# Performance work log

Measured on AMD Instinct MI355X. Metric: run time of the kernel, lower is better.

## Reference

```python
import jax, jax.numpy as jnp
import numpy as np

B, S, D, H, E, N = 4, 1024, 1024, 4096, 1024, 8


def setup_inputs() -> dict:
    key = jax.random.key(0)
    ks = jax.random.split(key, 5)
    x = jax.random.normal(ks[0], (B, S, D), jnp.float32)
    # Learned parameters (Linear weights stored as [in, out] for x @ W)
    Wg = jax.random.normal(ks[1], (D, N), jnp.float32) * 0.02
    bg = jnp.zeros((N,), jnp.float32)
    W1 = jax.random.normal(ks[2], (N, D, H), jnp.float32) * 0.02
    b1 = jnp.zeros((N, H), jnp.float32)
    W2 = jax.random.normal(ks[3], (N, H, E), jnp.float32) * 0.02
    b2 = jnp.zeros((N, E), jnp.float32)
    return {"x": x, "Wg": Wg, "bg": bg, "W1": W1, "b1": b1,
            "W2": W2, "b2": b2, "num_experts_per_tok": 2}


def reference(x, Wg, bg, W1, b1, W2, b2, num_experts_per_tok):
    # Gating: softmax over experts
    gate_probs = jax.nn.softmax(x @ Wg + bg, axis=-1)            # [B,S,N]
    n_exp = gate_probs.shape[-1]
    # Top-k routing mask (indices are distinct, so summed one-hots == scatter of 1.0)
    _, topk_idx = jax.lax.top_k(gate_probs, num_experts_per_tok)  # [B,S,k]
    mask = jax.nn.one_hot(topk_idx, n_exp, dtype=gate_probs.dtype).sum(axis=-2)  # [B,S,N]
    gated = gate_probs * mask
    # F.normalize(p=1): divide by max(L1-norm, eps)
    gated = gated / jnp.maximum(jnp.sum(jnp.abs(gated), axis=-1, keepdims=True), 1e-12)
    # Dense all-expert FFN (matches torch.stack over ModuleList)
    h = jax.nn.relu(jnp.einsum('bsd,ndh->bsnh', x, W1) + b1)      # [B,S,N,H]
    expert_out = jnp.einsum('bsnh,nhe->bsne', h, W2) + b2          # [B,S,N,E]
    out = jnp.einsum('bsn,bsne->bse', gated, expert_out)           # [B,S,E]
    # Auxiliary load-balancing stats
    tokens = float(x.shape[0] * x.shape[1])
    importance = gate_probs.sum(axis=(0, 1)) / tokens              # [N]
    load = mask.sum(axis=(0, 1)) / tokens                          # [N]
    lb_loss = (n_exp * (importance * load).sum()).astype(out.dtype)
    return out, lb_loss, importance, load
```

## Files before the change

kernel.cpp:

```cpp
#include <hip/hip_runtime.h>

#define TOKENS 4096
#define DDIM 1024
#define HDIM 4096
#define EDIM 1024
#define NEXP 8
#define SLOTS (TOKENS * 2)
#define OUT_MAIN ((size_t)TOKENS * EDIM)
#define NKC2 2
#define KCHUNK2 (HDIM / NKC2)

typedef __bf16 bf16_t;
typedef bf16_t bf16x8 __attribute__((ext_vector_type(8)));
typedef float f32x4 __attribute__((ext_vector_type(4)));

__device__ __forceinline__ unsigned short f32_to_bf16(float f) {
  union { float f; unsigned u; } v; v.f = f;
  unsigned r = v.u + 0x7FFFu + ((v.u >> 16) & 1u);
  return (unsigned short)(r >> 16);
}

__device__ __forceinline__ void gload_lds16(const void* g, void* l) {
  __builtin_amdgcn_global_load_lds(
      (__attribute__((address_space(1))) void*)(g),
      (__attribute__((address_space(3))) void*)(l), 16, 0, 0);
}

__global__ __launch_bounds__(256) void gate_kernel(
    const float* __restrict__ x, const float* __restrict__ Wg,
    const float* __restrict__ bg, unsigned short* __restrict__ xb,
    int2* __restrict__ tok_e, float2* __restrict__ tok_w,
    float* __restrict__ probs) {
  const int wave = threadIdx.x >> 6;
  const int lane = threadIdx.x & 63;
  const int t = blockIdx.x * 4 + wave;
  const float4* xr = reinterpret_cast<const float4*>(x + (size_t)t * DDIM);
  ushort4* xbr = reinterpret_cast<ushort4*>(xb + (size_t)t * DDIM);

  float acc[NEXP];
#pragma unroll
  for (int n = 0; n < NEXP; n++) acc[n] = 0.f;

#pragma unroll
  for (int i = 0; i < 4; i++) {
    int d4 = lane + 64 * i;
    float4 xv = xr[d4];
    ushort4 o;
    o.x = f32_to_bf16(xv.x); o.y = f32_to_bf16(xv.y);
    o.z = f32_to_bf16(xv.z); o.w = f32_to_bf16(xv.w);
    xbr[d4] = o;
    const float* wrow = Wg + (size_t)d4 * 4 * NEXP;
#pragma unroll
    for (int n = 0; n < NEXP; n++)
      acc[n] += xv.x * wrow[n] + xv.y * wrow[NEXP + n] +
                xv.z * wrow[2 * NEXP + n] + xv.w * wrow[3 * NEXP + n];
  }
#pragma unroll
  for (int n = 0; n < NEXP; n++)
#pragma unroll
    for (int m = 32; m > 0; m >>= 1) acc[n] += __shfl_xor(acc[n], m, 64);

  if (lane == 0) {
    float p[NEXP];
    float mx = -1e30f;
#pragma unroll
    for (int n = 0; n < NEXP; n++) { p[n] = acc[n] + bg[n]; mx = fmaxf(mx, p[n]); }
    float s = 0.f;
#pragma unroll
    for (int n = 0; n < NEXP; n++) { p[n] = expf(p[n] - mx); s += p[n]; }
    float inv = 1.f / s;
#pragma unroll
    for (int n = 0; n < NEXP; n++) { p[n] *= inv; probs[(size_t)t * NEXP + n] = p[n]; }
    int e1 = 0; float p1 = p[0];
#pragma unroll
    for (int n = 1; n < NEXP; n++) if (p[n] > p1) { p1 = p[n]; e1 = n; }
    int e2 = (e1 == 0) ? 1 : 0; float p2 = p[e2];
#pragma unroll
    for (int n = 0; n < NEXP; n++) if (n != e1 && p[n] > p2) { p2 = p[n]; e2 = n; }
    float denom = p1 + p2;
    tok_e[t] = make_int2(e1, e2);
    tok_w[t] = make_float2(p1 / denom, p2 / denom);
  }
}

__global__ __launch_bounds__(1024) void route_kernel(
    const int2* __restrict__ tok_e, const float2* __restrict__ tok_w,
    int* __restrict__ offs_g, int* __restrict__ counts_g,
    int* __restrict__ token_ids, float* __restrict__ slot_w) {
  __shared__ int cnt[NEXP];
  __shared__ int offs[NEXP + 1];
  __shared__ int cur[NEXP];
  const int tid = threadIdx.x;
  if (tid < NEXP) cnt[tid] = 0;
  __syncthreads();
  int2 e[4]; float2 w[4];
#pragma unroll
  for (int i = 0; i < 4; i++) {
    int t = tid + 1024 * i;
    e[i] = tok_e[t]; w[i] = tok_w[t];
    atomicAdd(&cnt[e[i].x], 1);
    atomicAdd(&cnt[e[i].y], 1);
  }
  __syncthreads();
  if (tid == 0) {
    int s = 0;
#pragma unroll
    for (int n = 0; n < NEXP; n++) { offs[n] = s; cur[n] = s; s += cnt[n]; }
    offs[NEXP] = s;
  }
  __syncthreads();
  if (tid < NEXP) { offs_g[tid] = offs[tid]; counts_g[tid] = cnt[tid]; }
  if (tid == 0) offs_g[NEXP] = offs[NEXP];
#pragma unroll
  for (int i = 0; i < 4; i++) {
    int t = tid + 1024 * i;
    int s0 = atomicAdd(&cur[e[i].x], 1);
    token_ids[s0] = t; slot_w[s0] = w[i].x;
    int s1 = atomicAdd(&cur[e[i].y], 1);
    token_ids[s1] = t; slot_w[s1] = w[i].y;
  }
}

__global__ __launch_bounds__(256) void transpose_convert_kernel(
    const float* __restrict__ src, unsigned short* __restrict__ dst, int R, int C) {
  __shared__ float tile[64][65];
  const size_t mat = (size_t)R * C;
  const float* s = src + (size_t)blockIdx.z * mat;
  unsigned short* d = dst + (size_t)blockIdx.z * mat;
  int c0 = blockIdx.x * 64, r0 = blockIdx.y * 64;
  int tx = threadIdx.x & 15, ty = threadIdx.x >> 4;
#pragma unroll
  for (int i = 0; i < 4; i++) {
    int row = ty + 16 * i;
    float4 v = *reinterpret_cast<const float4*>(&s[(size_t)(r0 + row) * C + c0 + tx * 4]);
    tile[row][tx * 4 + 0] = v.x;
    tile[row][tx * 4 + 1] = v.y;
    tile[row][tx * 4 + 2] = v.z;
    tile[row][tx * 4 + 3] = v.w;
  }
  __syncthreads();
#pragma unroll
  for (int i = 0; i < 4; i++) {
    int col = ty + 16 * i;
    ushort4 o;
    o.x = f32_to_bf16(tile[tx * 4 + 0][col]);
    o.y = f32_to_bf16(tile[tx * 4 + 1][col]);
    o.z = f32_to_bf16(tile[tx * 4 + 2][col]);
    o.w = f32_to_bf16(tile[tx * 4 + 3][col]);
    *reinterpret_cast<ushort4*>(&d[(size_t)(c0 + col) * R + r0 + tx * 4]) = o;
  }
}

__global__ __launch_bounds__(256) void gemm1_kernel(
    const unsigned short* __restrict__ xb, const unsigned short* __restrict__ w1t,
    const float* __restrict__ b1, const int* __restrict__ token_ids,
    const int* __restrict__ offs, unsigned short* __restrict__ h) {
  const int e = blockIdx.z;
  const int off0 = offs[e];
  const int ne = offs[e + 1] - off0;
  const int mt = blockIdx.y;
  if (mt * 128 >= ne) return;
  const int nt = blockIdx.x;

  __shared__ unsigned short As[2][128 * 64];
  __shared__ unsigned short Bs[2][128 * 64];

  const int tid = threadIdx.x;
  const int lane = tid & 63;
  const int wave = tid >> 6;
  const int wm = (wave >> 1) * 64;
  const int wn = (wave & 1) * 64;

  const int prow = tid >> 3;
  const int krow = (tid & 7) ^ (prow & 7);
  const unsigned short* gA[4];
  const unsigned short* gB[4];
  const unsigned short* wbase = w1t + (size_t)e * HDIM * DDIM;
#pragma unroll
  for (int j = 0; j < 4; j++) {
    int row = prow + j * 32;
    int slot = off0 + min(mt * 128 + row, ne - 1);
    gA[j] = xb + (size_t)token_ids[slot] * DDIM + krow * 8;
    gB[j] = wbase + (size_t)(nt * 128 + row) * DDIM + krow * 8;
  }

  f32x4 acc[4][4];
#pragma unroll
  for (int i = 0; i < 4; i++)
#pragma unroll
    for (int j = 0; j < 4; j++) acc[i][j] = (f32x4)(0.f);

  const int frow = lane & 15;
  const int q = lane >> 4;
  const int NK = DDIM / 64;

  auto stage = [&](int tt, int buf) {
#pragma unroll
    for (int j = 0; j < 4; j++) {
      gload_lds16(gA[j] + tt * 64, &As[buf][j * 2048 + wave * 512]);
      gload_lds16(gB[j] + tt * 64, &Bs[buf][j * 2048 + wave * 512]);
    }
  };

  stage(0, 0);
  stage(1, 1);

  for (int t = 0; t < NK; t++) {
    const int cur = t & 1;
    if (t == NK - 1) asm volatile("s_waitcnt vmcnt(0)" ::: "memory");
    else             asm volatile("s_waitcnt vmcnt(8)" ::: "memory");
    __builtin_amdgcn_s_barrier();

    bf16x8 af[2][4], bfv[2][4];
#pragma unroll
    for (int kk = 0; kk < 2; kk++) {
#pragma unroll
      for (int mi = 0; mi < 4; mi++) {
        int row = wm + mi * 16 + frow;
        int k16 = (kk * 4 + q) ^ (row & 7);
        af[kk][mi] = *reinterpret_cast<const bf16x8*>(&As[cur][row * 64 + k16 * 8]);
      }
#pragma unroll
      for (int ni = 0; ni < 4; ni++) {
        int row = wn + ni * 16 + frow;
        int k16 = (kk * 4 + q) ^ (row & 7);
        bfv[kk][ni] = *reinterpret_cast<const bf16x8*>(&Bs[cur][row * 64 + k16 * 8]);
      }
    }
    asm volatile("s_waitcnt lgkmcnt(0)" ::: "memory");
    __builtin_amdgcn_s_barrier();
    if (t + 2 < NK) stage(t + 2, cur);

    __builtin_amdgcn_s_setprio(1);
#pragma unroll
    for (int kk = 0; kk < 2; kk++)
#pragma unroll
      for (int mi = 0; mi < 4; mi++)
#pragma unroll
        for (int ni = 0; ni < 4; ni++)
          acc[mi][ni] = __builtin_amdgcn_mfma_f32_16x16x32_bf16(af[kk][mi], bfv[kk][ni], acc[mi][ni], 0, 0, 0);
    __builtin_amdgcn_s_setprio(0);
  }

  const float* b1e = b1 + (size_t)e * HDIM + nt * 128;
  const int r4 = (lane >> 4) * 4;
  const int cb = lane & 15;
#pragma unroll
  for (int mi = 0; mi < 4; mi++) {
#pragma unroll
    for (int r = 0; r < 4; r++) {
      int grow = mt * 128 + wm + mi * 16 + r4 + r;
      if (grow < ne) {
        unsigned short* hr = h + (size_t)(off0 + grow) * HDIM + nt * 128;
#pragma unroll
        for (int ni = 0; ni < 4; ni++) {
          int col = wn + ni * 16 + cb;
          float v = acc[mi][ni][r] + b1e[col];
          hr[col] = f32_to_bf16(fmaxf(v, 0.f));
        }
      }
    }
  }
}

__global__ __launch_bounds__(256) void gemm2_kernel(
    const unsigned short* __restrict__ h, const unsigned short* __restrict__ w2t,
    const float* __restrict__ b2, const int* __restrict__ token_ids,
    const float* __restrict__ slot_w, const int* __restrict__ offs,
    float* __restrict__ out) {
  const int ez = blockIdx.z;
  const int e = ez >> 1;
  const int kc = ez & 1;
  const int off0 = offs[e];
  const int ne = offs[e + 1] - off0;
  const int mt = blockIdx.y;
  if (mt * 128 >= ne) return;
  const int nt = blockIdx.x;

  __shared__ unsigned short As[2][128 * 64];
  __shared__ unsigned short Bs[2][128 * 64];

  const int tid = threadIdx.x;
  const int lane = tid & 63;
  const int wave = tid >> 6;
  const int wm = (wave >> 1) * 64;
  const int wn = (wave & 1) * 64;

  const int prow = tid >> 3;
  const int krow = (tid & 7) ^ (prow & 7);
  const unsigned short* gA[4];
  const unsigned short* gB[4];
  const unsigned short* wbase = w2t + (size_t)e * EDIM * HDIM;
  const int kbase = kc * KCHUNK2;
#pragma unroll
  for (int j = 0; j < 4; j++) {
    int row = prow + j * 32;
    int slot = off0 + min(mt * 128 + row, ne - 1);
    gA[j] = h + (size_t)slot * HDIM + kbase + krow * 8;
    gB[j] = wbase + (size_t)(nt * 128 + row) * HDIM + kbase + krow * 8;
  }

  f32x4 acc[4][4];
#pragma unroll
  for (int i = 0; i < 4; i++)
#pragma unroll
    for (int j = 0; j < 4; j++) acc[i][j] = (f32x4)(0.f);

  const int frow = lane & 15;
  const int q = lane >> 4;
  const int NK = KCHUNK2 / 64;

  auto stage = [&](int tt, int buf) {
#pragma unroll
    for (int j = 0; j < 4; j++) {
      gload_lds16(gA[j] + tt * 64, &As[buf][j * 2048 + wave * 512]);
      gload_lds16(gB[j] + tt * 64, &Bs[buf][j * 2048 + wave * 512]);
    }
  };

  stage(0, 0);
  stage(1, 1);

  for (int t = 0; t < NK; t++) {
    const int cur = t & 1;
    if (t == NK - 1) asm volatile("s_waitcnt vmcnt(0)" ::: "memory");
    else             asm volatile("s_waitcnt vmcnt(8)" ::: "memory");
    __builtin_amdgcn_s_barrier();

    bf16x8 af[2][4], bfv[2][4];
#pragma unroll
    for (int kk = 0; kk < 2; kk++) {
#pragma unroll
      for (int mi = 0; mi < 4; mi++) {
        int row = wm + mi * 16 + frow;
        int k16 = (kk * 4 + q) ^ (row & 7);
        af[kk][mi] = *reinterpret_cast<const bf16x8*>(&As[cur][row * 64 + k16 * 8]);
      }
#pragma unroll
      for (int ni = 0; ni < 4; ni++) {
        int row = wn + ni * 16 + frow;
        int k16 = (kk * 4 + q) ^ (row & 7);
        bfv[kk][ni] = *reinterpret_cast<const bf16x8*>(&Bs[cur][row * 64 + k16 * 8]);
      }
    }
    asm volatile("s_waitcnt lgkmcnt(0)" ::: "memory");
    __builtin_amdgcn_s_barrier();
    if (t + 2 < NK) stage(t + 2, cur);

    __builtin_amdgcn_s_setprio(1);
#pragma unroll
    for (int kk = 0; kk < 2; kk++)
#pragma unroll
      for (int mi = 0; mi < 4; mi++)
#pragma unroll
        for (int ni = 0; ni < 4; ni++)
          acc[mi][ni] = __builtin_amdgcn_mfma_f32_16x16x32_bf16(af[kk][mi], bfv[kk][ni], acc[mi][ni], 0, 0, 0);
    __builtin_amdgcn_s_setprio(0);
  }

  const float* b2e = b2 + (size_t)e * EDIM + nt * 128;
  const int r4 = (lane >> 4) * 4;
  const int cb = lane & 15;
#pragma unroll
  for (int mi = 0; mi < 4; mi++) {
#pragma unroll
    for (int r = 0; r < 4; r++) {
      int grow = mt * 128 + wm + mi * 16 + r4 + r;
      if (grow < ne) {
        int slot = off0 + grow;
        int tokid = token_ids[slot];
        float wgt = slot_w[slot];
        float* orow = out + (size_t)tokid * EDIM + nt * 128;
#pragma unroll
        for (int ni = 0; ni < 4; ni++) {
          int col = wn + ni * 16 + cb;
          float bias = (kc == 0) ? b2e[col] : 0.f;
          atomicAdd(&orow[col], (acc[mi][ni][r] + bias) * wgt);
        }
      }
    }
  }
}

__global__ __launch_bounds__(512) void stats_kernel(
    const float* __restrict__ probs, const int* __restrict__ counts,
    float* __restrict__ tail) {
  const int wave = threadIdx.x >> 6;
  const int lane = threadIdx.x & 63;
  float s = 0.f;
  for (int t = lane; t < TOKENS; t += 64) s += probs[(size_t)t * NEXP + wave];
#pragma unroll
  for (int m = 32; m > 0; m >>= 1) s += __shfl_xor(s, m, 64);
  __shared__ float imp_s[NEXP];
  if (lane == 0) imp_s[wave] = s / (float)TOKENS;
  __syncthreads();
  if (threadIdx.x == 0) {
    float lb = 0.f;
#pragma unroll
    for (int n = 0; n < NEXP; n++) {
      float imp = imp_s[n];
      float ld = (float)counts[n] / (float)TOKENS;
      tail[1 + n] = imp;
      tail[1 + NEXP + n] = ld;
      lb += imp * ld;
    }
    tail[0] = (float)NEXP * lb;
  }
}

extern "C" void kernel_launch(void* const* d_in, const int* in_sizes, int n_in,
                              void* d_out, int out_size, void* d_ws, size_t ws_size,
                              hipStream_t stream) {
  const float* x  = (const float*)d_in[0];
  const float* Wg = (const float*)d_in[1];
  const float* bg = (const float*)d_in[2];
  const float* W1 = (const float*)d_in[3];
  const float* b1 = (const float*)d_in[4];
  const float* W2 = (const float*)d_in[5];
  const float* b2 = (const float*)d_in[6];
  float* out = (float*)d_out;
  char* ws = (char*)d_ws;

  const size_t XB_OFF   = 0;
  const size_t W1T_OFF  = XB_OFF + (size_t)TOKENS * DDIM * 2;
  const size_t W2T_OFF  = W1T_OFF + (size_t)NEXP * DDIM * HDIM * 2;
  const size_t H_OFF    = W2T_OFF + (size_t)NEXP * HDIM * EDIM * 2;
  const size_t TOKE_OFF = H_OFF + (size_t)SLOTS * HDIM * 2;
  const size_t TOKW_OFF = TOKE_OFF + (size_t)TOKENS * sizeof(int2);
  const size_t TID_OFF  = TOKW_OFF + (size_t)TOKENS * sizeof(float2);
  const size_t SLW_OFF  = TID_OFF + (size_t)SLOTS * 4;
  const size_t PROB_OFF = SLW_OFF + (size_t)SLOTS * 4;
  const size_t META_OFF = PROB_OFF + (size_t)TOKENS * NEXP * 4;
  const size_t WS_NEED  = META_OFF + 64 * 4;
  if (ws_size < WS_NEED) return;

  unsigned short* xb   = (unsigned short*)(ws + XB_OFF);
  unsigned short* w1t  = (unsigned short*)(ws + W1T_OFF);
  unsigned short* w2t  = (unsigned short*)(ws + W2T_OFF);
  unsigned short* hbuf = (unsigned short*)(ws + H_OFF);
  int2*   tok_e = (int2*)(ws + TOKE_OFF);
  float2* tok_w = (float2*)(ws + TOKW_OFF);
  int*    tids  = (int*)(ws + TID_OFF);
  float*  slw   = (float*)(ws + SLW_OFF);
  float*  probs = (float*)(ws + PROB_OFF);
  int*    counts = (int*)(ws + META_OFF);
  int*    offs   = counts + 8;

  hipMemsetAsync(out, 0, (size_t)out_size * sizeof(float), stream);

  gate_kernel<<<TOKENS / 4, 256, 0, stream>>>(x, Wg, bg, xb, tok_e, tok_w, probs);
  route_kernel<<<1, 1024, 0, stream>>>(tok_e, tok_w, offs, counts, tids, slw);
  transpose_convert_kernel<<<dim3(HDIM / 64, DDIM / 64, NEXP), 256, 0, stream>>>(W1, w1t, DDIM, HDIM);
  transpose_convert_kernel<<<dim3(EDIM / 64, HDIM / 64, NEXP), 256, 0, stream>>>(W2, w2t, HDIM, EDIM);
  gemm1_kernel<<<dim3(HDIM / 128, SLOTS / 128, NEXP), 256, 0, stream>>>(xb, w1t, b1, tids, offs, hbuf);
  gemm2_kernel<<<dim3(EDIM / 128, SLOTS / 128, NEXP * NKC2), 256, 0, stream>>>(hbuf, w2t, b2, tids, slw, offs, out);
  stats_kernel<<<1, 512, 0, stream>>>(probs, counts, out + OUT_MAIN);
}
```

Measured before the change: 436.4 us.

## Enlarge grouped GEMM tiles to 256x256 with 8 waves and interleaved fragment loads

Both expert GEMMs move from 128x128 tiles with 4 waves to 256x256 tiles with 8 waves, each wave covering 128x64. Shared memory grows to 128KB per block, and launch bounds are set to one block per CU. The inner loop now loads B fragments once and then streams A fragments in groups interleaved with MFMAs, which keeps register pressure down for the doubled accumulators. The goal is higher arithmetic intensity and less global/LDS traffic per FLOP. The costs are fewer blocks, which gives worse wave quantization and more padding waste on per-expert M tails, and gemm2 gets only 4 N-tiles.

```diff
diff --git a/kernel.cpp b/kernel.cpp
--- a/kernel.cpp
+++ b/kernel.cpp
@@ -151,7 +151,8 @@
   }
 }
 
-__global__ __launch_bounds__(256) void gemm1_kernel(
+
+__global__ __launch_bounds__(512, 1) void gemm1_kernel(
     const unsigned short* __restrict__ xb, const unsigned short* __restrict__ w1t,
     const float* __restrict__ b1, const int* __restrict__ token_ids,
     const int* __restrict__ offs, unsigned short* __restrict__ h) {
@@ -159,17 +160,17 @@
   const int off0 = offs[e];
   const int ne = offs[e + 1] - off0;
   const int mt = blockIdx.y;
-  if (mt * 128 >= ne) return;
+  if (mt * 256 >= ne) return;
   const int nt = blockIdx.x;
 
-  __shared__ unsigned short As[2][128 * 64];
-  __shared__ unsigned short Bs[2][128 * 64];
+  __shared__ unsigned short As[2][256 * 64];
+  __shared__ unsigned short Bs[2][256 * 64];
 
   const int tid = threadIdx.x;
   const int lane = tid & 63;
   const int wave = tid >> 6;
-  const int wm = (wave >> 1) * 64;
-  const int wn = (wave & 1) * 64;
+  const int wm = (wave >> 2) * 128;
+  const int wn = (wave & 3) * 64;
 
   const int prow = tid >> 3;
   const int krow = (tid & 7) ^ (prow & 7);
@@ -178,15 +179,15 @@
   const unsigned short* wbase = w1t + (size_t)e * HDIM * DDIM;
 #pragma unroll
   for (int j = 0; j < 4; j++) {
-    int row = prow + j * 32;
-    int slot = off0 + min(mt * 128 + row, ne - 1);
+    int row = prow + j * 64;
+    int slot = off0 + min(mt * 256 + row, ne - 1);
     gA[j] = xb + (size_t)token_ids[slot] * DDIM + krow * 8;
-    gB[j] = wbase + (size_t)(nt * 128 + row) * DDIM + krow * 8;
-  }
-
-  f32x4 acc[4][4];
-#pragma unroll
-  for (int i = 0; i < 4; i++)
+    gB[j] = wbase + (size_t)(nt * 256 + row) * DDIM + krow * 8;
+  }
+
+  f32x4 acc[8][4];
+#pragma unroll
+  for (int i = 0; i < 8; i++)
 #pragma unroll
     for (int j = 0; j < 4; j++) acc[i][j] = (f32x4)(0.f);
 
@@ -197,8 +198,8 @@
   auto stage = [&](int tt, int buf) {
 #pragma unroll
     for (int j = 0; j < 4; j++) {
-      gload_lds16(gA[j] + tt * 64, &As[buf][j * 2048 + wave * 512]);
-      gload_lds16(gB[j] + tt * 64, &Bs[buf][j * 2048 + wave * 512]);
+      gload_lds16(gA[j] + tt * 64, &As[buf][j * 4096 + wave * 512]);
+      gload_lds16(gB[j] + tt * 64, &Bs[buf][j * 4096 + wave * 512]);
     }
   };
 
@@ -211,47 +212,53 @@
     else             asm volatile("s_waitcnt vmcnt(8)" ::: "memory");
     __builtin_amdgcn_s_barrier();
 
-    bf16x8 af[2][4], bfv[2][4];
-#pragma unroll
-    for (int kk = 0; kk < 2; kk++) {
-#pragma unroll
-      for (int mi = 0; mi < 4; mi++) {
-        int row = wm + mi * 16 + frow;
-        int k16 = (kk * 4 + q) ^ (row & 7);
-        af[kk][mi] = *reinterpret_cast<const bf16x8*>(&As[cur][row * 64 + k16 * 8]);
-      }
-#pragma unroll
-      for (int ni = 0; ni < 4; ni++) {
+    __builtin_amdgcn_s_setprio(1);
+    bf16x8 bfv[4][2];
+#pragma unroll
+    for (int ni = 0; ni < 4; ni++)
+#pragma unroll
+      for (int kk = 0; kk < 2; kk++) {
         int row = wn + ni * 16 + frow;
         int k16 = (kk * 4 + q) ^ (row & 7);
-        bfv[kk][ni] = *reinterpret_cast<const bf16x8*>(&Bs[cur][row * 64 + k16 * 8]);
+        bfv[ni][kk] = *reinterpret_cast<const bf16x8*>(&Bs[cur][row * 64 + k16 * 8]);
       }
-    }
+#pragma unroll
+    for (int g = 0; g < 4; g++) {
+      bf16x8 af[2][2];
+#pragma unroll
+      for (int m2 = 0; m2 < 2; m2++)
+#pragma unroll
+        for (int kk = 0; kk < 2; kk++) {
+          int row = wm + (g * 2 + m2) * 16 + frow;
+          int k16 = (kk * 4 + q) ^ (row & 7);
+          af[m2][kk] = *reinterpret_cast<const bf16x8*>(&As[cur][row * 64 + k16 * 8]);
+        }
+#pragma unroll
+      for (int m2 = 0; m2 < 2; m2++)
+#pragma unroll
+        for (int ni = 0; ni < 4; ni++)
+#pragma unroll
+          for (int kk = 0; kk < 2; kk++)
+            acc[g * 2 + m2][ni] = __builtin_amdgcn_mfma_f32_16x16x32_bf16(
+                af[m2][kk], bfv[ni][kk], acc[g * 2 + m2][ni], 0, 0, 0);
+    }
+    __builtin_amdgcn_s_setprio(0);
+
     asm volatile("s_waitcnt lgkmcnt(0)" ::: "memory");
     __builtin_amdgcn_s_barrier();
     if (t + 2 < NK) stage(t + 2, cur);
-
-    __builtin_amdgcn_s_setprio(1);
-#pragma unroll
-    for (int kk = 0; kk < 2; kk++)
-#pragma unroll
-      for (int mi = 0; mi < 4; mi++)
-#pragma unroll
-        for (int ni = 0; ni < 4; ni++)
-          acc[mi][ni] = __builtin_amdgcn_mfma_f32_16x16x32_bf16(af[kk][mi], bfv[kk][ni], acc[mi][ni], 0, 0, 0);
-    __builtin_amdgcn_s_setprio(0);
-  }
-
-  const float* b1e = b1 + (size_t)e * HDIM + nt * 128;
+  }
+
+  const float* b1e = b1 + (size_t)e * HDIM + nt * 256;
   const int r4 = (lane >> 4) * 4;
   const int cb = lane & 15;
 #pragma unroll
-  for (int mi = 0; mi < 4; mi++) {
+  for (int mi = 0; mi < 8; mi++) {
 #pragma unroll
     for (int r = 0; r < 4; r++) {
-      int grow = mt * 128 + wm + mi * 16 + r4 + r;
+      int grow = mt * 256 + wm + mi * 16 + r4 + r;
       if (grow < ne) {
-        unsigned short* hr = h + (size_t)(off0 + grow) * HDIM + nt * 128;
+        unsigned short* hr = h + (size_t)(off0 + grow) * HDIM + nt * 256;
 #pragma unroll
         for (int ni = 0; ni < 4; ni++) {
           int col = wn + ni * 16 + cb;
@@ -263,7 +270,7 @@
   }
 }
 
-__global__ __launch_bounds__(256) void gemm2_kernel(
+__global__ __launch_bounds__(512, 1) void gemm2_kernel(
     const unsigned short* __restrict__ h, const unsigned short* __restrict__ w2t,
     const float* __restrict__ b2, const int* __restrict__ token_ids,
     const float* __restrict__ slot_w, const int* __restrict__ offs,
@@ -274,17 +281,17 @@
   const int off0 = offs[e];
   const int ne = offs[e + 1] - off0;
   const int mt = blockIdx.y;
-  if (mt * 128 >= ne) return;
+  if (mt * 256 >= ne) return;
   const int nt = blockIdx.x;
 
-  __shared__ unsigned short As[2][128 * 64];
-  __shared__ unsigned short Bs[2][128 * 64];
+  __shared__ unsigned short As[2][256 * 64];
+  __shared__ unsigned short Bs[2][256 * 64];
 
   const int tid = threadIdx.x;
   const int lane = tid & 63;
   const int wave = tid >> 6;
-  const int wm = (wave >> 1) * 64;
-  const int wn = (wave & 1) * 64;
+  const int wm = (wave >> 2) * 128;
+  const int wn = (wave & 3) * 64;
 
   const int prow = tid >> 3;
   const int krow = (tid & 7) ^ (prow & 7);
@@ -294,15 +301,15 @@
   const int kbase = kc * KCHUNK2;
 #pragma unroll
   for (int j = 0; j < 4; j++) {
-    int row = prow + j * 32;
-    int slot = off0 + min(mt * 128 + row, ne - 1);
+    int row = prow + j * 64;
+    int slot = off0 + min(mt * 256 + row, ne - 1);
     gA[j] = h + (size_t)slot * HDIM + kbase + krow * 8;
-    gB[j] = wbase + (size_t)(nt * 128 + row) * HDIM + kbase + krow * 8;
-  }
-
-  f32x4 acc[4][4];
-#pragma unroll
-  for (int i = 0; i < 4; i++)
+    gB[j] = wbase + (size_t)(nt * 256 + row) * HDIM + kbase + krow * 8;
+  }
+
+  f32x4 acc[8][4];
+#pragma unroll
+  for (int i = 0; i < 8; i++)
 #pragma unroll
     for (int j = 0; j < 4; j++) acc[i][j] = (f32x4)(0.f);
 
@@ -313,8 +320,8 @@
   auto stage = [&](int tt, int buf) {
 #pragma unroll
     for (int j = 0; j < 4; j++) {
-      gload_lds16(gA[j] + tt * 64, &As[buf][j * 2048 + wave * 512]);
-      gload_lds16(gB[j] + tt * 64, &Bs[buf][j * 2048 + wave * 512]);
+      gload_lds16(gA[j] + tt * 64, &As[buf][j * 4096 + wave * 512]);
+      gload_lds16(gB[j] + tt * 64, &Bs[buf][j * 4096 + wave * 512]);
     }
   };
 
@@ -327,50 +334,56 @@
     else             asm volatile("s_waitcnt vmcnt(8)" ::: "memory");
     __builtin_amdgcn_s_barrier();
 
-    bf16x8 af[2][4], bfv[2][4];
-#pragma unroll
-    for (int kk = 0; kk < 2; kk++) {
-#pragma unroll
-      for (int mi = 0; mi < 4; mi++) {
-        int row = wm + mi * 16 + frow;
-        int k16 = (kk * 4 + q) ^ (row & 7);
-        af[kk][mi] = *reinterpret_cast<const bf16x8*>(&As[cur][row * 64 + k16 * 8]);
-      }
-#pragma unroll
-      for (int ni = 0; ni < 4; ni++) {
+    __builtin_amdgcn_s_setprio(1);
+    bf16x8 bfv[4][2];
+#pragma unroll
+    for (int ni = 0; ni < 4; ni++)
+#pragma unroll
+      for (int kk = 0; kk < 2; kk++) {
         int row = wn + ni * 16 + frow;
         int k16 = (kk * 4 + q) ^ (row & 7);
-        bfv[kk][ni] = *reinterpret_cast<const bf16x8*>(&Bs[cur][row * 64 + k16 * 8]);
+        bfv[ni][kk] = *reinterpret_cast<const bf16x8*>(&Bs[cur][row * 64 + k16 * 8]);
       }
-    }
+#pragma unroll
+    for (int g = 0; g < 4; g++) {
+      bf16x8 af[2][2];
+#pragma unroll
+      for (int m2 = 0; m2 < 2; m2++)
+#pragma unroll
+        for (int kk = 0; kk < 2; kk++) {
+          int row = wm + (g * 2 + m2) * 16 + frow;
+          int k16 = (kk * 4 + q) ^ (row & 7);
+          af[m2][kk] = *reinterpret_cast<const bf16x8*>(&As[cur][row * 64 + k16 * 8]);
+        }
+#pragma unroll
+      for (int m2 = 0; m2 < 2; m2++)
+#pragma unroll
+        for (int ni = 0; ni < 4; ni++)
+#pragma unroll
+          for (int kk = 0; kk < 2; kk++)
+            acc[g * 2 + m2][ni] = __builtin_amdgcn_mfma_f32_16x16x32_bf16(
+                af[m2][kk], bfv[ni][kk], acc[g * 2 + m2][ni], 0, 0, 0);
+    }
+    __builtin_amdgcn_s_setprio(0);
+
     asm volatile("s_waitcnt lgkmcnt(0)" ::: "memory");
     __builtin_amdgcn_s_barrier();
     if (t + 2 < NK) stage(t + 2, cur);
-
-    __builtin_amdgcn_s_setprio(1);
-#pragma unroll
-    for (int kk = 0; kk < 2; kk++)
-#pragma unroll
-      for (int mi = 0; mi < 4; mi++)
-#pragma unroll
-        for (int ni = 0; ni < 4; ni++)
-          acc[mi][ni] = __builtin_amdgcn_mfma_f32_16x16x32_bf16(af[kk][mi], bfv[kk][ni], acc[mi][ni], 0, 0, 0);
-    __builtin_amdgcn_s_setprio(0);
-  }
-
-  const float* b2e = b2 + (size_t)e * EDIM + nt * 128;
+  }
+
+  const float* b2e = b2 + (size_t)e * EDIM + nt * 256;
   const int r4 = (lane >> 4) * 4;
   const int cb = lane & 15;
 #pragma unroll
-  for (int mi = 0; mi < 4; mi++) {
+  for (int mi = 0; mi < 8; mi++) {
 #pragma unroll
     for (int r = 0; r < 4; r++) {
-      int grow = mt * 128 + wm + mi * 16 + r4 + r;
+      int grow = mt * 256 + wm + mi * 16 + r4 + r;
       if (grow < ne) {
         int slot = off0 + grow;
         int tokid = token_ids[slot];
         float wgt = slot_w[slot];
-        float* orow = out + (size_t)tokid * EDIM + nt * 128;
+        float* orow = out + (size_t)tokid * EDIM + nt * 256;
 #pragma unroll
         for (int ni = 0; ni < 4; ni++) {
           int col = wn + ni * 16 + cb;
@@ -452,7 +465,7 @@
   route_kernel<<<1, 1024, 0, stream>>>(tok_e, tok_w, offs, counts, tids, slw);
   transpose_convert_kernel<<<dim3(HDIM / 64, DDIM / 64, NEXP), 256, 0, stream>>>(W1, w1t, DDIM, HDIM);
   transpose_convert_kernel<<<dim3(EDIM / 64, HDIM / 64, NEXP), 256, 0, stream>>>(W2, w2t, HDIM, EDIM);
-  gemm1_kernel<<<dim3(HDIM / 128, SLOTS / 128, NEXP), 256, 0, stream>>>(xb, w1t, b1, tids, offs, hbuf);
-  gemm2_kernel<<<dim3(EDIM / 128, SLOTS / 128, NEXP * NKC2), 256, 0, stream>>>(hbuf, w2t, b2, tids, slw, offs, out);
+  gemm1_kernel<<<dim3(HDIM / 256, SLOTS / 256, NEXP), 512, 0, stream>>>(xb, w1t, b1, tids, offs, hbuf);
+  gemm2_kernel<<<dim3(EDIM / 256, SLOTS / 256, NEXP * NKC2), 512, 0, stream>>>(hbuf, w2t, b2, tids, slw, offs, out);
   stats_kernel<<<1, 512, 0, stream>>>(probs, counts, out + OUT_MAIN);
 }
```

Measured after the change: 524.5 us. 1.2x slower.

## Remap GEMM workgroups per XCD and interleave LDS fragment loads with MFMAs

Applied to the files above, without the earlier changes.

Both grouped GEMM kernels now launch a 1D grid and remap block IDs so that consecutive logical tiles (same expert and M tile) land on the same XCD. This is meant to improve L2 reuse of A and B tiles across the chiplets. The inner loop also loads B fragments once per k-step and A fragments in pairs, issuing MFMAs between the loads. That lowers register pressure and overlaps LDS reads with compute, but it moves the LDS reads to after the barrier and before the next stage, so the prefetch now waits for the compute to finish.

```diff
diff --git a/kernel.cpp b/kernel.cpp
--- a/kernel.cpp
+++ b/kernel.cpp
@@ -9,6 +9,14 @@
 #define OUT_MAIN ((size_t)TOKENS * EDIM)
 #define NKC2 2
 #define KCHUNK2 (HDIM / NKC2)
+
+#define G1_NT (HDIM / 128)
+#define G1_MT (SLOTS / 128)
+#define G1_NWG (G1_NT * G1_MT * NEXP)
+#define G2_NT (EDIM / 128)
+#define G2_MT (SLOTS / 128)
+#define G2_NWG (G2_NT * G2_MT * NEXP * NKC2)
+#define NXCD 8
 
 typedef __bf16 bf16_t;
 typedef bf16_t bf16x8 __attribute__((ext_vector_type(8)));
@@ -151,16 +159,20 @@
   }
 }
 
+
 __global__ __launch_bounds__(256) void gemm1_kernel(
     const unsigned short* __restrict__ xb, const unsigned short* __restrict__ w1t,
     const float* __restrict__ b1, const int* __restrict__ token_ids,
     const int* __restrict__ offs, unsigned short* __restrict__ h) {
-  const int e = blockIdx.z;
+  const int hw = blockIdx.x;
+  const int l = (hw & (NXCD - 1)) * (G1_NWG / NXCD) + (hw >> 3);
+  const int nt = l & (G1_NT - 1);
+  const int mt = (l >> 5) & (G1_MT - 1);
+  const int e  = l >> 11;
+
   const int off0 = offs[e];
   const int ne = offs[e + 1] - off0;
-  const int mt = blockIdx.y;
   if (mt * 128 >= ne) return;
-  const int nt = blockIdx.x;
 
   __shared__ unsigned short As[2][128 * 64];
   __shared__ unsigned short Bs[2][128 * 64];
@@ -211,35 +223,35 @@
     else             asm volatile("s_waitcnt vmcnt(8)" ::: "memory");
     __builtin_amdgcn_s_barrier();
 
-    bf16x8 af[2][4], bfv[2][4];
+    __builtin_amdgcn_s_setprio(1);
 #pragma unroll
     for (int kk = 0; kk < 2; kk++) {
-#pragma unroll
-      for (int mi = 0; mi < 4; mi++) {
-        int row = wm + mi * 16 + frow;
-        int k16 = (kk * 4 + q) ^ (row & 7);
-        af[kk][mi] = *reinterpret_cast<const bf16x8*>(&As[cur][row * 64 + k16 * 8]);
-      }
+      bf16x8 bfv[4];
 #pragma unroll
       for (int ni = 0; ni < 4; ni++) {
         int row = wn + ni * 16 + frow;
         int k16 = (kk * 4 + q) ^ (row & 7);
-        bfv[kk][ni] = *reinterpret_cast<const bf16x8*>(&Bs[cur][row * 64 + k16 * 8]);
-      }
-    }
+        bfv[ni] = *reinterpret_cast<const bf16x8*>(&Bs[cur][row * 64 + k16 * 8]);
+      }
+#pragma unroll
+      for (int mp = 0; mp < 2; mp++) {
+        bf16x8 af0, af1;
+        { int row = wm + (mp * 2) * 16 + frow;     int k16 = (kk * 4 + q) ^ (row & 7);
+          af0 = *reinterpret_cast<const bf16x8*>(&As[cur][row * 64 + k16 * 8]); }
+        { int row = wm + (mp * 2 + 1) * 16 + frow; int k16 = (kk * 4 + q) ^ (row & 7);
+          af1 = *reinterpret_cast<const bf16x8*>(&As[cur][row * 64 + k16 * 8]); }
+#pragma unroll
+        for (int ni = 0; ni < 4; ni++) {
+          acc[mp * 2][ni]     = __builtin_amdgcn_mfma_f32_16x16x32_bf16(af0, bfv[ni], acc[mp * 2][ni], 0, 0, 0);
+          acc[mp * 2 + 1][ni] = __builtin_amdgcn_mfma_f32_16x16x32_bf16(af1, bfv[ni], acc[mp * 2 + 1][ni], 0, 0, 0);
+        }
+      }
+    }
+    __builtin_amdgcn_s_setprio(0);
+
     asm volatile("s_waitcnt lgkmcnt(0)" ::: "memory");
     __builtin_amdgcn_s_barrier();
     if (t + 2 < NK) stage(t + 2, cur);
-
-    __builtin_amdgcn_s_setprio(1);
-#pragma unroll
-    for (int kk = 0; kk < 2; kk++)
-#pragma unroll
-      for (int mi = 0; mi < 4; mi++)
-#pragma unroll
-        for (int ni = 0; ni < 4; ni++)
-          acc[mi][ni] = __builtin_amdgcn_mfma_f32_16x16x32_bf16(af[kk][mi], bfv[kk][ni], acc[mi][ni], 0, 0, 0);
-    __builtin_amdgcn_s_setprio(0);
   }
 
   const float* b1e = b1 + (size_t)e * HDIM + nt * 128;
@@ -268,14 +280,17 @@
     const float* __restrict__ b2, const int* __restrict__ token_ids,
     const float* __restrict__ slot_w, const int* __restrict__ offs,
     float* __restrict__ out) {
-  const int ez = blockIdx.z;
+  const int hw = blockIdx.x;
+  const int l = (hw & (NXCD - 1)) * (G2_NWG / NXCD) + (hw >> 3);
+  const int nt = l & (G2_NT - 1);
+  const int mt = (l >> 3) & (G2_MT - 1);
+  const int ez = l >> 9;
   const int e = ez >> 1;
   const int kc = ez & 1;
+
   const int off0 = offs[e];
   const int ne = offs[e + 1] - off0;
-  const int mt = blockIdx.y;
   if (mt * 128 >= ne) return;
-  const int nt = blockIdx.x;
 
   __shared__ unsigned short As[2][128 * 64];
   __shared__ unsigned short Bs[2][128 * 64];
@@ -327,35 +342,35 @@
     else             asm volatile("s_waitcnt vmcnt(8)" ::: "memory");
     __builtin_amdgcn_s_barrier();
 
-    bf16x8 af[2][4], bfv[2][4];
+    __builtin_amdgcn_s_setprio(1);
 #pragma unroll
     for (int kk = 0; kk < 2; kk++) {
-#pragma unroll
-      for (int mi = 0; mi < 4; mi++) {
-        int row = wm + mi * 16 + frow;
-        int k16 = (kk * 4 + q) ^ (row & 7);
-        af[kk][mi] = *reinterpret_cast<const bf16x8*>(&As[cur][row * 64 + k16 * 8]);
-      }
+      bf16x8 bfv[4];
 #pragma unroll
       for (int ni = 0; ni < 4; ni++) {
         int row = wn + ni * 16 + frow;
         int k16 = (kk * 4 + q) ^ (row & 7);
-        bfv[kk][ni] = *reinterpret_cast<const bf16x8*>(&Bs[cur][row * 64 + k16 * 8]);
-      }
-    }
+        bfv[ni] = *reinterpret_cast<const bf16x8*>(&Bs[cur][row * 64 + k16 * 8]);
+      }
+#pragma unroll
+      for (int mp = 0; mp < 2; mp++) {
+        bf16x8 af0, af1;
+        { int row = wm + (mp * 2) * 16 + frow;     int k16 = (kk * 4 + q) ^ (row & 7);
+          af0 = *reinterpret_cast<const bf16x8*>(&As[cur][row * 64 + k16 * 8]); }
+        { int row = wm + (mp * 2 + 1) * 16 + frow; int k16 = (kk * 4 + q) ^ (row & 7);
+          af1 = *reinterpret_cast<const bf16x8*>(&As[cur][row * 64 + k16 * 8]); }
+#pragma unroll
+        for (int ni = 0; ni < 4; ni++) {
+          acc[mp * 2][ni]     = __builtin_amdgcn_mfma_f32_16x16x32_bf16(af0, bfv[ni], acc[mp * 2][ni], 0, 0, 0);
+          acc[mp * 2 + 1][ni] = __builtin_amdgcn_mfma_f32_16x16x32_bf16(af1, bfv[ni], acc[mp * 2 + 1][ni], 0, 0, 0);
+        }
+      }
+    }
+    __builtin_amdgcn_s_setprio(0);
+
     asm volatile("s_waitcnt lgkmcnt(0)" ::: "memory");
     __builtin_amdgcn_s_barrier();
     if (t + 2 < NK) stage(t + 2, cur);
-
-    __builtin_amdgcn_s_setprio(1);
-#pragma unroll
-    for (int kk = 0; kk < 2; kk++)
-#pragma unroll
-      for (int mi = 0; mi < 4; mi++)
-#pragma unroll
-        for (int ni = 0; ni < 4; ni++)
-          acc[mi][ni] = __builtin_amdgcn_mfma_f32_16x16x32_bf16(af[kk][mi], bfv[kk][ni], acc[mi][ni], 0, 0, 0);
-    __builtin_amdgcn_s_setprio(0);
   }
 
   const float* b2e = b2 + (size_t)e * EDIM + nt * 128;
@@ -452,7 +467,7 @@
   route_kernel<<<1, 1024, 0, stream>>>(tok_e, tok_w, offs, counts, tids, slw);
   transpose_convert_kernel<<<dim3(HDIM / 64, DDIM / 64, NEXP), 256, 0, stream>>>(W1, w1t, DDIM, HDIM);
   transpose_convert_kernel<<<dim3(EDIM / 64, HDIM / 64, NEXP), 256, 0, stream>>>(W2, w2t, HDIM, EDIM);
-  gemm1_kernel<<<dim3(HDIM / 128, SLOTS / 128, NEXP), 256, 0, stream>>>(xb, w1t, b1, tids, offs, hbuf);
-  gemm2_kernel<<<dim3(EDIM / 128, SLOTS / 128, NEXP * NKC2), 256, 0, stream>>>(hbuf, w2t, b2, tids, slw, offs, out);
+  gemm1_kernel<<<G1_NWG, 256, 0, stream>>>(xb, w1t, b1, tids, offs, hbuf);
+  gemm2_kernel<<<G2_NWG, 256, 0, stream>>>(hbuf, w2t, b2, tids, slw, offs, out);
   stats_kernel<<<1, 512, 0, stream>>>(probs, counts, out + OUT_MAIN);
 }
```

New measurement: 459.9 us. 1.05x slower.
